# Optimization experiments

Measured on AMD Instinct MI355X. Metric: run time of the kernel, lower is better.

Reference implementation:

```python
import jax, jax.numpy as jnp
import numpy as np

GAMMA = 0.96875      # retention decay, 1 - 2**-5
GROUPS = 8           # config.group_norm_num
EPS = 1e-6           # config.retention_group_norm_eps


def _get_D(T, dtype):
    # D[n, m] = gamma**(n-m) for n >= m else 0 (causal exponential decay)
    n = jnp.arange(T)[:, None]
    m = jnp.arange(T)[None, :]
    log_g = jnp.log(jnp.asarray(GAMMA, dtype))
    # where-select avoids inf*0 NaNs for n < m (matches D[D != D] = 0)
    return jnp.where(n >= m, jnp.exp((n - m).astype(dtype) * log_g),
                     jnp.zeros((), dtype))


def _group_norm(x, w, b):
    # x: (N, C); torch.nn.GroupNorm semantics (biased variance, affine)
    N, C = x.shape
    xg = x.reshape(N, GROUPS, C // GROUPS)
    mu = xg.mean(-1, keepdims=True)
    var = xg.var(-1, keepdims=True)
    xn = ((xg - mu) * jax.lax.rsqrt(var + EPS)).reshape(N, C)
    return xn * w + b


def setup_inputs() -> dict:
    key = jax.random.key(0)
    k0, k1, k2, k3, k4 = jax.random.split(key, 5)
    B, T, C = 2, 8192, 64
    Q_in = jax.random.normal(k0, (B, T, C), jnp.float32)
    W_Q = jax.random.normal(k1, (C, C), jnp.float32) / C
    W_K = jax.random.normal(k2, (C, C), jnp.float32) / C
    W_V = jax.random.normal(k3, (C, C), jnp.float32) / C
    gn_weight = 1.0 + 0.02 * jax.random.normal(k4, (C,), jnp.float32)
    gn_bias = jnp.zeros((C,), jnp.float32)
    return {"Q_in": Q_in, "W_Q": W_Q, "W_K": W_K, "W_V": W_V,
            "gn_weight": gn_weight, "gn_bias": gn_bias}


def reference(Q_in, W_Q, W_K, W_V, gn_weight, gn_bias):
    B, T, C = Q_in.shape
    # _qkv with KV_in=None, act='none'
    Q = Q_in @ W_Q
    K = Q_in @ W_K
    V = Q_in @ W_V
    # retention scores with multiplicative causal decay mask
    QK = jnp.einsum("btc,bsc->bts", Q, K) * _get_D(T, Q.dtype)[None]
    out = jnp.einsum("bts,bsc->btc", QK, V)  # (B, T, C)
    # _out: dropout(p=0) -> GroupNorm over flattened (B*T, C) -> transpose+view
    out = _group_norm(out.reshape(-1, C), gn_weight, gn_bias).reshape(B, T, C)
    out = jnp.swapaxes(out, -2, -1).reshape(B, T, C)  # faithful to .transpose().view()
    return out
```

## Files before the change

kernel.cpp:

```cpp
#include <hip/hip_runtime.h>


constexpr int SEQ = 8192;
constexpr int CH  = 64;
constexpr float LOG2G = -0.045803690f;

typedef __attribute__((ext_vector_type(8))) _Float16 half8;
typedef __attribute__((ext_vector_type(4))) float    f32x4;

__device__ inline unsigned short f2h(float x) {
    _Float16 h = (_Float16)x;
    return __builtin_bit_cast(unsigned short, h);
}

__global__ __launch_bounds__(256) void qkv_kernel(
    const float* __restrict__ Xin, const float* __restrict__ Wq,
    const float* __restrict__ Wk, const float* __restrict__ Wv,
    unsigned short* __restrict__ Qh, unsigned short* __restrict__ Kh,
    unsigned short* __restrict__ Vt)
{
    __shared__ unsigned short sWt[3][64][72];
    const int tid = threadIdx.x;
    const size_t row0 = (size_t)blockIdx.x * 64;
    const int b  = (int)(row0 >> 13);
    const int t0 = (int)(row0 & (SEQ - 1));

    {
        const int c  = tid & 63;
        const int k0 = (tid >> 6) * 2;
        #pragma unroll
        for (int m = 0; m < 3; ++m) {
            const float* W = (m == 0) ? Wq : ((m == 1) ? Wk : Wv);
            #pragma unroll
            for (int it = 0; it < 8; ++it) {
                const int k = k0 + it * 8;
                const unsigned lo = f2h(W[k * 64 + c]);
                const unsigned hi = f2h(W[(k + 1) * 64 + c]);
                *(unsigned int*)&sWt[m][c][k] = lo | (hi << 16);
            }
        }
    }

    const int l15 = tid & 15, q4 = (tid >> 4) & 3, wvi = tid >> 6;

    half8 xf[2];
    {
        const float* Xp = Xin + (row0 + (size_t)(wvi * 16 + l15)) * 64;
        #pragma unroll
        for (int h = 0; h < 2; ++h) {
            const f32x4 a  = *(const f32x4*)(Xp + h * 32 + q4 * 8);
            const f32x4 bb = *(const f32x4*)(Xp + h * 32 + q4 * 8 + 4);
            half8 t;
            t[0] = (_Float16)a[0];  t[1] = (_Float16)a[1];
            t[2] = (_Float16)a[2];  t[3] = (_Float16)a[3];
            t[4] = (_Float16)bb[0]; t[5] = (_Float16)bb[1];
            t[6] = (_Float16)bb[2]; t[7] = (_Float16)bb[3];
            xf[h] = t;
        }
    }
    __syncthreads();

    const int trow = (int)row0 + wvi * 16;
    #pragma unroll
    for (int m = 0; m < 2; ++m) {
        unsigned short* O = (m == 0) ? Qh : Kh;
        #pragma unroll
        for (int ct = 0; ct < 4; ++ct) {
            const half8 wf0 = *(const half8*)&sWt[m][ct * 16 + l15][q4 * 8];
            const half8 wf1 = *(const half8*)&sWt[m][ct * 16 + l15][32 + q4 * 8];
            f32x4 d = {0.f, 0.f, 0.f, 0.f};
            d = __builtin_amdgcn_mfma_f32_16x16x32_f16(xf[0], wf0, d, 0, 0, 0);
            d = __builtin_amdgcn_mfma_f32_16x16x32_f16(xf[1], wf1, d, 0, 0, 0);
            #pragma unroll
            for (int i = 0; i < 4; ++i)
                O[(size_t)(trow + q4 * 4 + i) * 64 + ct * 16 + l15] = f2h(d[i]);
        }
    }
    #pragma unroll
    for (int mt = 0; mt < 4; ++mt) {
        const half8 wf0 = *(const half8*)&sWt[2][mt * 16 + l15][q4 * 8];
        const half8 wf1 = *(const half8*)&sWt[2][mt * 16 + l15][32 + q4 * 8];
        f32x4 d = {0.f, 0.f, 0.f, 0.f};
        d = __builtin_amdgcn_mfma_f32_16x16x32_f16(wf0, xf[0], d, 0, 0, 0);
        d = __builtin_amdgcn_mfma_f32_16x16x32_f16(wf1, xf[1], d, 0, 0, 0);
        #pragma unroll
        for (int i = 0; i < 4; ++i)
            Vt[(size_t)(b * 64 + mt * 16 + q4 * 4 + i) * SEQ + t0 + wvi * 16 + l15] = f2h(d[i]);
    }
}

__global__ __launch_bounds__(128, 2) void attn_kernel(
    const unsigned short* __restrict__ Qh, const unsigned short* __restrict__ Kh,
    const unsigned short* __restrict__ Vt,
    const float* __restrict__ gnw, const float* __restrict__ gnb,
    float* __restrict__ out)
{
    __shared__ unsigned short sS[2][16][88];
    __shared__ __align__(16) float sP[2][16][68];
    __shared__ float sGW[64], sGB[64];

    const int tid  = threadIdx.x;
    const int wvi  = tid >> 6;
    const int lane = tid & 63;
    const int l15  = lane & 15, q4 = lane >> 4;
    const int tile = blockIdx.x;
    const int b    = tile >> 9;
    const int t0   = (tile & 511) << 4;

    if (tid < 64) { sGW[tid] = gnw[tid]; sGB[tid] = gnb[tid]; }
    __syncthreads();

    const unsigned short* Qp = Qh + (size_t)(b * SEQ + t0 + l15) * 64 + q4 * 8;
    const half8 qf0 = *(const half8*)Qp;
    const half8 qf1 = *(const half8*)(Qp + 32);

    float grs[4][4];
    #pragma unroll
    for (int st = 0; st < 4; ++st) {
        #pragma unroll
        for (int i = 0; i < 4; ++i)
            grs[st][i] = exp2f((float)(l15 - (st * 16 + q4 * 4 + i)) * LOG2G);
    }

    f32x4 acc[4];
    #pragma unroll
    for (int ct = 0; ct < 4; ++ct) acc[ct] = (f32x4){0.f, 0.f, 0.f, 0.f};

    const int cs_hi = (t0 + 15) >> 6;
    const int cs_lo = (cs_hi >= 10) ? (cs_hi - 9) : 0;
    const int n     = cs_hi - cs_lo + 1;
    const int n0    = n >> 1;
    const int myLo  = cs_lo + (wvi ? n0 : 0);
    const int myHi  = wvi ? cs_hi : (cs_lo + n0 - 1);

    const unsigned short* Kbase = Kh + (size_t)b * SEQ * 64;
    const unsigned short* Vbase = Vt + (size_t)b * 64 * SEQ;

    half8 kA[4][2], vA[4][2], kB[4][2], vB[4][2];

    auto loadKV = [&](int cs, half8 (&kf)[4][2], half8 (&vf)[4][2]) {
        const int s0 = cs << 6;
        #pragma unroll
        for (int st = 0; st < 4; ++st) {
            const unsigned short* p = Kbase + (size_t)(s0 + st * 16 + l15) * 64 + q4 * 8;
            kf[st][0] = *(const half8*)p;
            kf[st][1] = *(const half8*)(p + 32);
        }
        #pragma unroll
        for (int ct = 0; ct < 4; ++ct) {
            const unsigned short* p = Vbase + (size_t)(ct * 16 + l15) * SEQ + s0 + q4 * 8;
            vf[ct][0] = *(const half8*)p;
            vf[ct][1] = *(const half8*)(p + 32);
        }
    };

    auto body = [&](half8 (&kc)[4][2], half8 (&vc)[4][2],
                    half8 (&kn)[4][2], half8 (&vn)[4][2], int cs) {
        const int s0 = cs << 6;
        f32x4 sv[4];
        #pragma unroll
        for (int st = 0; st < 4; ++st) {
            f32x4 s = {0.f, 0.f, 0.f, 0.f};
            s = __builtin_amdgcn_mfma_f32_16x16x32_f16(kc[st][0], qf0, s, 0, 0, 0);
            s = __builtin_amdgcn_mfma_f32_16x16x32_f16(kc[st][1], qf1, s, 0, 0, 0);
            sv[st] = s;
        }
        if (cs < myHi) loadKV(cs + 1, kn, vn);
        const float gbase = exp2f((float)(t0 - s0) * LOG2G);
        if (s0 + 63 <= t0) {
            #pragma unroll
            for (int st = 0; st < 4; ++st) {
                const unsigned u0 = (unsigned)f2h(sv[st][0] * (gbase * grs[st][0]))
                                  | ((unsigned)f2h(sv[st][1] * (gbase * grs[st][1])) << 16);
                const unsigned u1 = (unsigned)f2h(sv[st][2] * (gbase * grs[st][2]))
                                  | ((unsigned)f2h(sv[st][3] * (gbase * grs[st][3])) << 16);
                unsigned int* p = (unsigned int*)&sS[wvi][l15][st * 16 + q4 * 4];
                p[0] = u0; p[1] = u1;
            }
        } else {
            const int dbase = t0 + l15 - s0;
            #pragma unroll
            for (int st = 0; st < 4; ++st) {
                float w[4];
                #pragma unroll
                for (int i = 0; i < 4; ++i) {
                    const int srel = st * 16 + q4 * 4 + i;
                    w[i] = (dbase - srel >= 0) ? gbase * grs[st][i] : 0.f;
                }
                const unsigned u0 = (unsigned)f2h(sv[st][0] * w[0])
                                  | ((unsigned)f2h(sv[st][1] * w[1]) << 16);
                const unsigned u1 = (unsigned)f2h(sv[st][2] * w[2])
                                  | ((unsigned)f2h(sv[st][3] * w[3]) << 16);
                unsigned int* p = (unsigned int*)&sS[wvi][l15][st * 16 + q4 * 4];
                p[0] = u0; p[1] = u1;
            }
        }
        const half8 af0 = *(const half8*)&sS[wvi][l15][q4 * 8];
        const half8 af1 = *(const half8*)&sS[wvi][l15][32 + q4 * 8];
        #pragma unroll
        for (int ct = 0; ct < 4; ++ct) {
            acc[ct] = __builtin_amdgcn_mfma_f32_16x16x32_f16(af0, vc[ct][0], acc[ct], 0, 0, 0);
            acc[ct] = __builtin_amdgcn_mfma_f32_16x16x32_f16(af1, vc[ct][1], acc[ct], 0, 0, 0);
        }
    };

    if (myLo <= myHi) {
        loadKV(myLo, kA, vA);
        int cs = myLo;
        while (true) {
            body(kA, vA, kB, vB, cs);
            if (++cs > myHi) break;
            body(kB, vB, kA, vA, cs);
            if (++cs > myHi) break;
        }
    }

    #pragma unroll
    for (int ct = 0; ct < 4; ++ct) {
        #pragma unroll
        for (int i = 0; i < 4; ++i)
            sP[wvi][q4 * 4 + i][ct * 16 + l15] = acc[ct][i];
    }
    __syncthreads();

    const int tt = (wvi << 3) | (lane >> 3);
    const int g  = lane & 7;
    float x[8];
    {
        const f32x4 a0 = *(const f32x4*)&sP[0][tt][g * 8];
        const f32x4 a1 = *(const f32x4*)&sP[0][tt][g * 8 + 4];
        const f32x4 b0 = *(const f32x4*)&sP[1][tt][g * 8];
        const f32x4 b1 = *(const f32x4*)&sP[1][tt][g * 8 + 4];
        #pragma unroll
        for (int j = 0; j < 4; ++j) { x[j] = a0[j] + b0[j]; x[4 + j] = a1[j] + b1[j]; }
    }
    float s = 0.f, ss = 0.f;
    #pragma unroll
    for (int j = 0; j < 8; ++j) { s += x[j]; ss += x[j] * x[j]; }
    const float mu  = s * 0.125f;
    const float var = ss * 0.125f - mu * mu;
    const float rs  = rsqrtf(var + 1e-6f);
    #pragma unroll
    for (int j = 0; j < 8; ++j) {
        const int c = g * 8 + j;
        x[j] = (x[j] - mu) * rs * sGW[c] + sGB[c];
    }
    *(f32x4*)&sP[0][tt][g * 8]     = (f32x4){x[0], x[1], x[2], x[3]};
    *(f32x4*)&sP[0][tt][g * 8 + 4] = (f32x4){x[4], x[5], x[6], x[7]};
    __syncthreads();

    #pragma unroll
    for (int k2 = 0; k2 < 8; ++k2) {
        const int c = ((wvi << 3) | k2) * 4 + q4;
        out[(size_t)(b * 64 + c) * SEQ + t0 + l15] = sP[0][l15][c];
    }
}

extern "C" void kernel_launch(void* const* d_in, const int* in_sizes, int n_in,
                              void* d_out, int out_size, void* d_ws, size_t ws_size,
                              hipStream_t stream)
{
    const float* Xin = (const float*)d_in[0];
    const float* Wq  = (const float*)d_in[1];
    const float* Wk  = (const float*)d_in[2];
    const float* Wv  = (const float*)d_in[3];
    const float* gnw = (const float*)d_in[4];
    const float* gnb = (const float*)d_in[5];

    const size_t NROW = (size_t)2 * SEQ;
    unsigned short* Qh = (unsigned short*)d_ws;
    unsigned short* Kh = Qh + NROW * CH;
    unsigned short* Vt = Kh + NROW * CH;

    qkv_kernel<<<dim3(256), dim3(256), 0, stream>>>(Xin, Wq, Wk, Wv, Qh, Kh, Vt);
    attn_kernel<<<dim3(1024), dim3(128), 0, stream>>>(Qh, Kh, Vt, gnw, gnb, (float*)d_out);
}
```

Measured before the change: 93.14 us.

## Split attention key range across four waves and vectorize Q/K stores

The attention kernel now launches 256 threads per block and splits each query tile's key chunks across four waves instead of two, reducing the serial chunk chain each wave walks. The cross-wave reduction and group norm are rewritten to sum four partial accumulators, with half the threads doing the normalization. Separately, the QKV kernel swaps MFMA operand order so each lane holds four consecutive channels and writes them as one 8-byte store instead of four scalar stores. The cost is more shared memory, more registers per block, and a larger reduction step.

```diff
diff --git a/kernel.cpp b/kernel.cpp
--- a/kernel.cpp
+++ b/kernel.cpp
@@ -65,15 +65,16 @@
     for (int m = 0; m < 2; ++m) {
         unsigned short* O = (m == 0) ? Qh : Kh;
         #pragma unroll
-        for (int ct = 0; ct < 4; ++ct) {
-            const half8 wf0 = *(const half8*)&sWt[m][ct * 16 + l15][q4 * 8];
-            const half8 wf1 = *(const half8*)&sWt[m][ct * 16 + l15][32 + q4 * 8];
+        for (int mt = 0; mt < 4; ++mt) {
+            const half8 wf0 = *(const half8*)&sWt[m][mt * 16 + l15][q4 * 8];
+            const half8 wf1 = *(const half8*)&sWt[m][mt * 16 + l15][32 + q4 * 8];
             f32x4 d = {0.f, 0.f, 0.f, 0.f};
-            d = __builtin_amdgcn_mfma_f32_16x16x32_f16(xf[0], wf0, d, 0, 0, 0);
-            d = __builtin_amdgcn_mfma_f32_16x16x32_f16(xf[1], wf1, d, 0, 0, 0);
-            #pragma unroll
-            for (int i = 0; i < 4; ++i)
-                O[(size_t)(trow + q4 * 4 + i) * 64 + ct * 16 + l15] = f2h(d[i]);
+            d = __builtin_amdgcn_mfma_f32_16x16x32_f16(wf0, xf[0], d, 0, 0, 0);
+            d = __builtin_amdgcn_mfma_f32_16x16x32_f16(wf1, xf[1], d, 0, 0, 0);
+            const unsigned u0 = (unsigned)f2h(d[0]) | ((unsigned)f2h(d[1]) << 16);
+            const unsigned u1 = (unsigned)f2h(d[2]) | ((unsigned)f2h(d[3]) << 16);
+            uint2 u; u.x = u0; u.y = u1;
+            *(uint2*)&O[(size_t)(trow + l15) * 64 + mt * 16 + q4 * 4] = u;
         }
     }
     #pragma unroll
@@ -89,14 +90,14 @@
     }
 }
 
-__global__ __launch_bounds__(128, 2) void attn_kernel(
+__global__ __launch_bounds__(256, 2) void attn_kernel(
     const unsigned short* __restrict__ Qh, const unsigned short* __restrict__ Kh,
     const unsigned short* __restrict__ Vt,
     const float* __restrict__ gnw, const float* __restrict__ gnb,
     float* __restrict__ out)
 {
-    __shared__ unsigned short sS[2][16][88];
-    __shared__ __align__(16) float sP[2][16][68];
+    __shared__ unsigned short sS[4][16][88];
+    __shared__ __align__(16) float sP[4][16][68];
     __shared__ float sGW[64], sGB[64];
 
     const int tid  = threadIdx.x;
@@ -129,9 +130,8 @@
     const int cs_hi = (t0 + 15) >> 6;
     const int cs_lo = (cs_hi >= 10) ? (cs_hi - 9) : 0;
     const int n     = cs_hi - cs_lo + 1;
-    const int n0    = n >> 1;
-    const int myLo  = cs_lo + (wvi ? n0 : 0);
-    const int myHi  = wvi ? cs_hi : (cs_lo + n0 - 1);
+    const int myLo  = cs_lo + (n * wvi) / 4;
+    const int myHi  = cs_lo + (n * (wvi + 1)) / 4 - 1;
 
     const unsigned short* Kbase = Kh + (size_t)b * SEQ * 64;
     const unsigned short* Vbase = Vt + (size_t)b * 64 * SEQ;
@@ -223,36 +223,41 @@
     }
     __syncthreads();
 
-    const int tt = (wvi << 3) | (lane >> 3);
-    const int g  = lane & 7;
-    float x[8];
-    {
-        const f32x4 a0 = *(const f32x4*)&sP[0][tt][g * 8];
-        const f32x4 a1 = *(const f32x4*)&sP[0][tt][g * 8 + 4];
-        const f32x4 b0 = *(const f32x4*)&sP[1][tt][g * 8];
-        const f32x4 b1 = *(const f32x4*)&sP[1][tt][g * 8 + 4];
-        #pragma unroll
-        for (int j = 0; j < 4; ++j) { x[j] = a0[j] + b0[j]; x[4 + j] = a1[j] + b1[j]; }
-    }
-    float s = 0.f, ss = 0.f;
-    #pragma unroll
-    for (int j = 0; j < 8; ++j) { s += x[j]; ss += x[j] * x[j]; }
-    const float mu  = s * 0.125f;
-    const float var = ss * 0.125f - mu * mu;
-    const float rs  = rsqrtf(var + 1e-6f);
-    #pragma unroll
-    for (int j = 0; j < 8; ++j) {
-        const int c = g * 8 + j;
-        x[j] = (x[j] - mu) * rs * sGW[c] + sGB[c];
-    }
-    *(f32x4*)&sP[0][tt][g * 8]     = (f32x4){x[0], x[1], x[2], x[3]};
-    *(f32x4*)&sP[0][tt][g * 8 + 4] = (f32x4){x[4], x[5], x[6], x[7]};
-    __syncthreads();
-
-    #pragma unroll
-    for (int k2 = 0; k2 < 8; ++k2) {
-        const int c = ((wvi << 3) | k2) * 4 + q4;
-        out[(size_t)(b * 64 + c) * SEQ + t0 + l15] = sP[0][l15][c];
+    if (tid < 128) {
+        const int tt = tid & 15;
+        const int g  = tid >> 4;
+        f32x4 v0 = *(const f32x4*)&sP[0][tt][g * 8];
+        f32x4 v1 = *(const f32x4*)&sP[0][tt][g * 8 + 4];
+        #pragma unroll
+        for (int w = 1; w < 4; ++w) {
+            const f32x4 a0 = *(const f32x4*)&sP[w][tt][g * 8];
+            const f32x4 a1 = *(const f32x4*)&sP[w][tt][g * 8 + 4];
+            #pragma unroll
+            for (int j = 0; j < 4; ++j) { v0[j] += a0[j]; v1[j] += a1[j]; }
+        }
+        float s = 0.f, ss = 0.f;
+        #pragma unroll
+        for (int j = 0; j < 4; ++j) {
+            s += v0[j] + v1[j]; ss += v0[j] * v0[j] + v1[j] * v1[j];
+        }
+        const float mu  = s * 0.125f;
+        const float var = ss * 0.125f - mu * mu;
+        const float rs  = rsqrtf(var + 1e-6f);
+        #pragma unroll
+        for (int j = 0; j < 4; ++j) {
+            const int c = g * 8 + j;
+            v0[j] = (v0[j] - mu) * rs * sGW[c] + sGB[c];
+            v1[j] = (v1[j] - mu) * rs * sGW[c + 4] + sGB[c + 4];
+        }
+        *(f32x4*)&sP[0][tt][g * 8]     = v0;
+        *(f32x4*)&sP[0][tt][g * 8 + 4] = v1;
+    }
+    __syncthreads();
+
+    #pragma unroll
+    for (int k = 0; k < 4; ++k) {
+        const int c = k * 16 + (tid >> 4);
+        out[(size_t)(b * 64 + c) * SEQ + t0 + (tid & 15)] = sP[0][tid & 15][c];
     }
 }
 
@@ -273,5 +278,5 @@
     unsigned short* Vt = Kh + NROW * CH;
 
     qkv_kernel<<<dim3(256), dim3(256), 0, stream>>>(Xin, Wq, Wk, Wv, Qh, Kh, Vt);
-    attn_kernel<<<dim3(1024), dim3(128), 0, stream>>>(Qh, Kh, Vt, gnw, gnb, (float*)d_out);
-}
+    attn_kernel<<<dim3(1024), dim3(256), 0, stream>>>(Qh, Kh, Vt, gnw, gnb, (float*)d_out);
+}
```

Measured after the change: 91.85 us. No clear change (-1.4%).
